# Kernel optimization log

Measured on AMD Instinct MI355X. Metric: run time of the kernel, lower is better.

## Reference

```python
import jax, jax.numpy as jnp
import numpy as np

B = 8192
D = 1024
NUM_CLASSES = 128
EPS = 1e-8  # torch F.cosine_similarity default eps


def setup_inputs() -> dict:
    key = jax.random.key(0)
    k1, k2, k3 = jax.random.split(key, 3)
    label_tensor = jax.random.randint(k1, (B,), 0, NUM_CLASSES, dtype=jnp.int64 if jax.config.jax_enable_x64 else jnp.int32)
    feature_a = jax.random.normal(k2, (B, D), dtype=jnp.float32)
    feature_b = jax.random.normal(k3, (B, D), dtype=jnp.float32)
    return {"label_tensor": label_tensor, "feature_a": feature_a, "feature_b": feature_b}


def reference(label_tensor, feature_a, feature_b):
    # Pairwise cosine similarity: cos_score[i, k] = cos(a_i, b_k), shape [B, B]
    dots = feature_a @ feature_b.T  # [B, B]
    na = jnp.linalg.norm(feature_a, axis=1)  # [B]
    nb = jnp.linalg.norm(feature_b, axis=1)  # [B]
    cos_score = dots / jnp.maximum(na[:, None] * nb[None, :], EPS)
    # Row-softmax (torch softmax dim=1 on the [B, B] matrix)
    logp = jax.nn.log_softmax(cos_score, axis=1)
    # Label-equality mask: positives for row i are all j with same label
    mask = (label_tensor[:, None] == label_tensor[None, :]).astype(cos_score.dtype)  # [B, B]
    per_row = -(mask * logp).sum(axis=1) / mask.sum(axis=1)  # diagonal guarantees >=1 positive
    loss = per_row.mean()
    return loss, cos_score
```

## Files before the change

### kernel.cpp

```cpp
#include <hip/hip_runtime.h>
#include <hip/hip_bf16.h>

#define NB 8192
#define ND 1024

typedef __bf16 bf16x8 __attribute__((ext_vector_type(8)));
typedef float  f32x4  __attribute__((ext_vector_type(4)));

__device__ inline void gload_lds16(const void* g, void* l) {
    __builtin_amdgcn_global_load_lds(
        (const __attribute__((address_space(1))) unsigned int*)g,
        (__attribute__((address_space(3))) unsigned int*)l,
        16, 0, 0);
}

__device__ inline unsigned short f2bf(float x) {
    unsigned int u = __float_as_uint(x);
    return (unsigned short)((u + 0x7fffu + ((u >> 16) & 1u)) >> 16);
}

#define BARRIER() asm volatile("s_barrier" ::: "memory")
#define VMCNT4()  asm volatile("s_waitcnt vmcnt(4)" ::: "memory")
#define VMCNT0()  asm volatile("s_waitcnt vmcnt(0)" ::: "memory")

__global__ __launch_bounds__(256) void prep_kernel(
    const float* __restrict__ A, const float* __restrict__ Bm,
    unsigned short* __restrict__ wa, unsigned short* __restrict__ wb,
    float* __restrict__ na, float* __restrict__ nb)
{
    int b = blockIdx.x;
    int wid = threadIdx.x >> 6, lane = threadIdx.x & 63;
    const float* src; unsigned short* dst; float* nrm; int row;
    if (b < 2048) { src = A;  dst = wa; nrm = na; row = b * 4 + wid; }
    else          { src = Bm; dst = wb; nrm = nb; row = (b - 2048) * 4 + wid; }

    const float*    rp = src + (size_t)row * ND;
    unsigned short* wp = dst + (size_t)row * ND;

    float ss = 0.f;
#pragma unroll
    for (int t = 0; t < 4; ++t) {
        int c = lane * 4 + t * 256;
        float4 v = *reinterpret_cast<const float4*>(rp + c);
        ss += v.x * v.x + v.y * v.y + v.z * v.z + v.w * v.w;
        ushort4 u;
        u.x = f2bf(v.x); u.y = f2bf(v.y); u.z = f2bf(v.z); u.w = f2bf(v.w);
        *reinterpret_cast<ushort4*>(wp + c) = u;
    }
#pragma unroll
    for (int off = 32; off; off >>= 1) ss += __shfl_xor(ss, off);
    if (lane == 0) nrm[row] = sqrtf(ss);
}

__global__ __launch_bounds__(256) void hist_kernel(
    const int* __restrict__ labels, int* __restrict__ hist)
{
    __shared__ int h[128];
    int tid = threadIdx.x;
    if (tid < 128) h[tid] = 0;
    __syncthreads();
    for (int i = tid; i < NB; i += 256) atomicAdd(&h[labels[i]], 1);
    __syncthreads();
    if (tid < 128) hist[tid] = h[tid];
}

__global__ __launch_bounds__(256) void gemm_cos(
    const unsigned short* __restrict__ wa, const unsigned short* __restrict__ wb,
    const float* __restrict__ na, const float* __restrict__ nb,
    const int* __restrict__ labels,
    float* __restrict__ C, float* __restrict__ pe, float* __restrict__ pm)
{
    __shared__ unsigned short lds[24576];

    const int bid = blockIdx.x;
    const int tm  = (bid & 7) * 8 + ((bid >> 3) & 7);
    const int tn  = bid >> 6;

    const int tid  = threadIdx.x;
    const int lane = tid & 63;
    const int wid  = tid >> 6;
    const int wr   = wid >> 1, wc = wid & 1;
    const int l15  = lane & 15, lg = lane >> 4;

    const int m0 = tm * 128, n0 = tn * 128;

    const int srow = tid >> 2;
    const int sg   = (tid & 3) ^ ((tid >> 3) & 3);
    const unsigned short* pA0 = wa + (size_t)(m0 + srow) * ND + sg * 8;
    const unsigned short* pA1 = pA0 + 64 * ND;
    const unsigned short* pB0 = wb + (size_t)(n0 + srow) * ND + sg * 8;
    const unsigned short* pB1 = pB0 + 64 * ND;
    const int stW = wid * 512;

    const int kg  = (lg ^ ((lane >> 1) & 3)) * 8;
    const int rdA = wr * 2048 + l15 * 32 + kg;
    const int rdB = 4096 + wc * 2048 + l15 * 32 + kg;

    f32x4 acc[4][4];
#pragma unroll
    for (int i = 0; i < 4; ++i)
#pragma unroll
        for (int j = 0; j < 4; ++j) acc[i][j] = (f32x4){0.f, 0.f, 0.f, 0.f};

#define STAGE(t, BUF) do { \
    gload_lds16(pA0 + (t) * 32, &lds[(BUF) + stW]); \
    gload_lds16(pA1 + (t) * 32, &lds[(BUF) + 2048 + stW]); \
    gload_lds16(pB0 + (t) * 32, &lds[(BUF) + 4096 + stW]); \
    gload_lds16(pB1 + (t) * 32, &lds[(BUF) + 6144 + stW]); } while (0)

#define COMPUTE(BUF) do { \
    bf16x8 bq[4], af[4]; \
    _Pragma("unroll") \
    for (int n_ = 0; n_ < 4; ++n_) \
        bq[n_] = *reinterpret_cast<const bf16x8*>(&lds[(BUF) + rdB + n_ * 512]); \
    _Pragma("unroll") \
    for (int m_ = 0; m_ < 4; ++m_) \
        af[m_] = *reinterpret_cast<const bf16x8*>(&lds[(BUF) + rdA + m_ * 512]); \
    _Pragma("unroll") \
    for (int m_ = 0; m_ < 4; ++m_) \
        _Pragma("unroll") \
        for (int n_ = 0; n_ < 4; ++n_) \
            acc[m_][n_] = __builtin_amdgcn_mfma_f32_16x16x32_bf16( \
                af[m_], bq[n_], acc[m_][n_], 0, 0, 0); \
    } while (0)

    STAGE(0, 0);
    STAGE(1, 8192);
    VMCNT4();
    BARRIER();

#pragma unroll
    for (int t = 0; t < 32; ++t) {
        const int cb  = (t % 3) * 8192;
        const int nb2 = ((t + 2) % 3) * 8192;
        if (t < 30) STAGE(t + 2, nb2);
        COMPUTE(cb);
        if (t < 29)      VMCNT4();
        else if (t < 31) VMCNT0();
        BARRIER();
    }

#undef COMPUTE
#undef STAGE

    __syncthreads();
    float* pl = reinterpret_cast<float*>(lds);

    float nbv[4]; int labc[4];
#pragma unroll
    for (int n = 0; n < 4; ++n) {
        int c = n0 + wc * 64 + n * 16 + l15;
        nbv[n] = nb[c]; labc[n] = labels[c];
    }

#pragma unroll
    for (int m = 0; m < 4; ++m) {
#pragma unroll
        for (int jj = 0; jj < 4; ++jj) {
            int rl = wr * 64 + m * 16 + lg * 4 + jj;
            int r  = m0 + rl;
            float nav = na[r]; int labr = labels[r];
            float es = 0.f, ms = 0.f;
#pragma unroll
            for (int n = 0; n < 4; ++n) {
                int c = n0 + wc * 64 + n * 16 + l15;
                float v = acc[m][n][jj] / fmaxf(nav * nbv[n], 1e-8f);
                C[(size_t)r * NB + c] = v;
                es += __expf(v);
                ms += (labc[n] == labr) ? v : 0.f;
            }
#pragma unroll
            for (int off = 1; off < 16; off <<= 1) {
                es += __shfl_xor(es, off);
                ms += __shfl_xor(ms, off);
            }
            if (l15 == 0) {
                int o = rl * 4 + wc * 2;
                pl[o] = es; pl[o + 1] = ms;
            }
        }
    }
    __syncthreads();
    if (tid < 128) {
        float es = pl[tid * 4]     + pl[tid * 4 + 2];
        float ms = pl[tid * 4 + 1] + pl[tid * 4 + 3];
        pe[tn * NB + m0 + tid] = es;
        pm[tn * NB + m0 + tid] = ms;
    }
}

__global__ __launch_bounds__(256) void loss_final(
    const float* __restrict__ pe, const float* __restrict__ pm,
    const int* __restrict__ labels, const int* __restrict__ hist,
    float* __restrict__ per_row)
{
    int row = blockIdx.x * 256 + threadIdx.x;
    float es = 0.f, ms = 0.f;
#pragma unroll
    for (int t = 0; t < 64; ++t) {
        es += pe[t * NB + row];
        ms += pm[t * NB + row];
    }
    per_row[row] = logf(es) - ms / (float)hist[labels[row]];
}

__global__ __launch_bounds__(256) void finalize(
    const float* __restrict__ per_row, float* __restrict__ out)
{
    __shared__ float sm[256];
    float s = 0.f;
    for (int i = threadIdx.x; i < NB; i += 256) s += per_row[i];
    sm[threadIdx.x] = s;
    __syncthreads();
    for (int k = 128; k; k >>= 1) {
        if (threadIdx.x < k) sm[threadIdx.x] += sm[threadIdx.x + k];
        __syncthreads();
    }
    if (threadIdx.x == 0) out[0] = sm[0] * (1.0f / (float)NB);
}

extern "C" void kernel_launch(void* const* d_in, const int* in_sizes, int n_in,
                              void* d_out, int out_size, void* d_ws, size_t ws_size,
                              hipStream_t stream) {
    const int*   labels = (const int*)d_in[0];
    const float* A      = (const float*)d_in[1];
    const float* Bm     = (const float*)d_in[2];
    float* out = (float*)d_out;

    char* ws = (char*)d_ws;
    unsigned short* wa = (unsigned short*)(ws);
    unsigned short* wb = (unsigned short*)(ws + 16777216);
    float* na      = (float*)(ws + 33554432);
    float* nb      = (float*)(ws + 33554432 + 32768);
    float* per_row = (float*)(ws + 33554432 + 65536);
    int*   hist    = (int*)  (ws + 33554432 + 98304);
    float* pe      = (float*)(ws + 33554432 + 131072);
    float* pm      = (float*)(ws + 33554432 + 131072 + 2097152);

    float* cosm = out + 1;

    prep_kernel<<<4096, 256, 0, stream>>>(A, Bm, wa, wb, na, nb);
    hist_kernel<<<1,    256, 0, stream>>>(labels, hist);
    gemm_cos   <<<4096, 256, 0, stream>>>(wa, wb, na, nb, labels, cosm, pe, pm);
    loss_final <<<32,   256, 0, stream>>>(pe, pm, labels, hist, per_row);
    finalize   <<<1,    256, 0, stream>>>(per_row, out);
}
```

Before: 271.7 us.

## Load B operand directly into registers from fragment-major pre-swizzled layout

The prep kernel now writes the bf16 copy of feature_b in a fragment-major layout that matches the MFMA B-operand, with 16-row by 8-element groups. The GEMM loads B fragments straight from global memory into double-buffered registers instead of staging them through LDS. Only A still goes through the triple-buffered LDS pipeline, which halves the shared-memory footprint. This removes the LDS writes and reads for B and may raise occupancy. In exchange, each wave issues redundant global loads for B that are shared across wave rows, and it relies on inline-asm waitcnt accounting.

```diff
diff --git a/kernel.cpp b/kernel.cpp
--- a/kernel.cpp
+++ b/kernel.cpp
@@ -5,6 +5,7 @@
 #define ND 1024
 
 typedef __bf16 bf16x8 __attribute__((ext_vector_type(8)));
+typedef int    i32x4  __attribute__((ext_vector_type(4)));
 typedef float  f32x4  __attribute__((ext_vector_type(4)));
 
 __device__ inline void gload_lds16(const void* g, void* l) {
@@ -14,28 +15,31 @@
         16, 0, 0);
 }
 
+__device__ inline void bload(const unsigned short* p, i32x4& d) {
+    asm volatile("global_load_dwordx4 %0, %1, off"
+                 : "=v"(d) : "v"(p) : "memory");
+}
+
 __device__ inline unsigned short f2bf(float x) {
     unsigned int u = __float_as_uint(x);
     return (unsigned short)((u + 0x7fffu + ((u >> 16) & 1u)) >> 16);
 }
 
 #define BARRIER() asm volatile("s_barrier" ::: "memory")
-#define VMCNT4()  asm volatile("s_waitcnt vmcnt(4)" ::: "memory")
+#define VMCNT6()  asm volatile("s_waitcnt vmcnt(6)" ::: "memory")
 #define VMCNT0()  asm volatile("s_waitcnt vmcnt(0)" ::: "memory")
+#define LGKM0()   asm volatile("s_waitcnt lgkmcnt(0)" ::: "memory")
 
 __global__ __launch_bounds__(256) void prep_kernel(
     const float* __restrict__ A, const float* __restrict__ Bm,
-    unsigned short* __restrict__ wa, unsigned short* __restrict__ wb,
+    unsigned short* __restrict__ wa, unsigned short* __restrict__ wb2,
     float* __restrict__ na, float* __restrict__ nb)
 {
     int b = blockIdx.x;
     int wid = threadIdx.x >> 6, lane = threadIdx.x & 63;
-    const float* src; unsigned short* dst; float* nrm; int row;
-    if (b < 2048) { src = A;  dst = wa; nrm = na; row = b * 4 + wid; }
-    else          { src = Bm; dst = wb; nrm = nb; row = (b - 2048) * 4 + wid; }
-
-    const float*    rp = src + (size_t)row * ND;
-    unsigned short* wp = dst + (size_t)row * ND;
+    bool isA = (b < 2048);
+    int row = (isA ? b : b - 2048) * 4 + wid;
+    const float* rp = (isA ? A : Bm) + (size_t)row * ND;
 
     float ss = 0.f;
 #pragma unroll
@@ -45,11 +49,17 @@
         ss += v.x * v.x + v.y * v.y + v.z * v.z + v.w * v.w;
         ushort4 u;
         u.x = f2bf(v.x); u.y = f2bf(v.y); u.z = f2bf(v.z); u.w = f2bf(v.w);
-        *reinterpret_cast<ushort4*>(wp + c) = u;
+        if (isA) {
+            *reinterpret_cast<ushort4*>(wa + (size_t)row * ND + c) = u;
+        } else {
+            size_t idx = (size_t)(row >> 4) * 16384 + (c >> 3) * 128
+                       + (row & 15) * 8 + (c & 7);
+            *reinterpret_cast<ushort4*>(wb2 + idx) = u;
+        }
     }
 #pragma unroll
     for (int off = 32; off; off >>= 1) ss += __shfl_xor(ss, off);
-    if (lane == 0) nrm[row] = sqrtf(ss);
+    if (lane == 0) (isA ? na : nb)[row] = sqrtf(ss);
 }
 
 __global__ __launch_bounds__(256) void hist_kernel(
@@ -65,12 +75,12 @@
 }
 
 __global__ __launch_bounds__(256) void gemm_cos(
-    const unsigned short* __restrict__ wa, const unsigned short* __restrict__ wb,
+    const unsigned short* __restrict__ wa, const unsigned short* __restrict__ wb2,
     const float* __restrict__ na, const float* __restrict__ nb,
     const int* __restrict__ labels,
     float* __restrict__ C, float* __restrict__ pe, float* __restrict__ pm)
 {
-    __shared__ unsigned short lds[24576];
+    __shared__ unsigned short lds[12288];
 
     const int bid = blockIdx.x;
     const int tm  = (bid & 7) * 8 + ((bid >> 3) & 7);
@@ -88,13 +98,13 @@
     const int sg   = (tid & 3) ^ ((tid >> 3) & 3);
     const unsigned short* pA0 = wa + (size_t)(m0 + srow) * ND + sg * 8;
     const unsigned short* pA1 = pA0 + 64 * ND;
-    const unsigned short* pB0 = wb + (size_t)(n0 + srow) * ND + sg * 8;
-    const unsigned short* pB1 = pB0 + 64 * ND;
     const int stW = wid * 512;
 
     const int kg  = (lg ^ ((lane >> 1) & 3)) * 8;
     const int rdA = wr * 2048 + l15 * 32 + kg;
-    const int rdB = 4096 + wc * 2048 + l15 * 32 + kg;
+
+    const unsigned short* qB = wb2 + (size_t)tn * 131072 + wc * 65536
+                             + lg * 128 + l15 * 8;
 
     f32x4 acc[4][4];
 #pragma unroll
@@ -102,46 +112,49 @@
 #pragma unroll
         for (int j = 0; j < 4; ++j) acc[i][j] = (f32x4){0.f, 0.f, 0.f, 0.f};
 
-#define STAGE(t, BUF) do { \
+    i32x4 breg[2][4];
+
+#define STAGE_A(t, BUF) do { \
     gload_lds16(pA0 + (t) * 32, &lds[(BUF) + stW]); \
-    gload_lds16(pA1 + (t) * 32, &lds[(BUF) + 2048 + stW]); \
-    gload_lds16(pB0 + (t) * 32, &lds[(BUF) + 4096 + stW]); \
-    gload_lds16(pB1 + (t) * 32, &lds[(BUF) + 6144 + stW]); } while (0)
-
-#define COMPUTE(BUF) do { \
-    bf16x8 bq[4], af[4]; \
-    _Pragma("unroll") \
+    gload_lds16(pA1 + (t) * 32, &lds[(BUF) + 2048 + stW]); } while (0)
+
+#define BLOAD(t, P) do { _Pragma("unroll") \
     for (int n_ = 0; n_ < 4; ++n_) \
-        bq[n_] = *reinterpret_cast<const bf16x8*>(&lds[(BUF) + rdB + n_ * 512]); \
-    _Pragma("unroll") \
-    for (int m_ = 0; m_ < 4; ++m_) \
-        af[m_] = *reinterpret_cast<const bf16x8*>(&lds[(BUF) + rdA + m_ * 512]); \
-    _Pragma("unroll") \
-    for (int m_ = 0; m_ < 4; ++m_) \
-        _Pragma("unroll") \
-        for (int n_ = 0; n_ < 4; ++n_) \
-            acc[m_][n_] = __builtin_amdgcn_mfma_f32_16x16x32_bf16( \
-                af[m_], bq[n_], acc[m_][n_], 0, 0, 0); \
-    } while (0)
-
-    STAGE(0, 0);
-    STAGE(1, 8192);
-    VMCNT4();
+        bload(qB + (t) * 512 + n_ * 16384, breg[P][n_]); } while (0)
+
+    STAGE_A(0, 0);
+    STAGE_A(1, 4096);
+    BLOAD(0, 0);
+    VMCNT6();
     BARRIER();
 
 #pragma unroll
     for (int t = 0; t < 32; ++t) {
-        const int cb  = (t % 3) * 8192;
-        const int nb2 = ((t + 2) % 3) * 8192;
-        if (t < 30) STAGE(t + 2, nb2);
-        COMPUTE(cb);
-        if (t < 29)      VMCNT4();
-        else if (t < 31) VMCNT0();
+        const int cb  = (t % 3) * 4096;
+        const int nb2 = ((t + 2) % 3) * 4096;
+        const int cp  = t & 1, np = cp ^ 1;
+        if (t < 30) STAGE_A(t + 2, nb2);
+        if (t < 31) BLOAD(t + 1, np);
+        bf16x8 af[4];
+#pragma unroll
+        for (int m_ = 0; m_ < 4; ++m_)
+            af[m_] = *reinterpret_cast<const bf16x8*>(&lds[cb + rdA + m_ * 512]);
+        if (t < 31) VMCNT6();
+        else        VMCNT0();
+        __builtin_amdgcn_sched_barrier(0);
+#pragma unroll
+        for (int m_ = 0; m_ < 4; ++m_)
+#pragma unroll
+            for (int n_ = 0; n_ < 4; ++n_)
+                acc[m_][n_] = __builtin_amdgcn_mfma_f32_16x16x32_bf16(
+                    af[m_], __builtin_bit_cast(bf16x8, breg[cp][n_]),
+                    acc[m_][n_], 0, 0, 0);
+        LGKM0();
         BARRIER();
     }
 
-#undef COMPUTE
-#undef STAGE
+#undef BLOAD
+#undef STAGE_A
 
     __syncthreads();
     float* pl = reinterpret_cast<float*>(lds);
@@ -228,8 +241,8 @@
     float* out = (float*)d_out;
 
     char* ws = (char*)d_ws;
-    unsigned short* wa = (unsigned short*)(ws);
-    unsigned short* wb = (unsigned short*)(ws + 16777216);
+    unsigned short* wa  = (unsigned short*)(ws);
+    unsigned short* wb2 = (unsigned short*)(ws + 16777216);
     float* na      = (float*)(ws + 33554432);
     float* nb      = (float*)(ws + 33554432 + 32768);
     float* per_row = (float*)(ws + 33554432 + 65536);
@@ -239,9 +252,9 @@
 
     float* cosm = out + 1;
 
-    prep_kernel<<<4096, 256, 0, stream>>>(A, Bm, wa, wb, na, nb);
+    prep_kernel<<<4096, 256, 0, stream>>>(A, Bm, wa, wb2, na, nb);
     hist_kernel<<<1,    256, 0, stream>>>(labels, hist);
-    gemm_cos   <<<4096, 256, 0, stream>>>(wa, wb, na, nb, labels, cosm, pe, pm);
+    gemm_cos   <<<4096, 256, 0, stream>>>(wa, wb2, na, nb, labels, cosm, pe, pm);
     loss_final <<<32,   256, 0, stream>>>(pe, pm, labels, hist, per_row);
     finalize   <<<1,    256, 0, stream>>>(per_row, out);
 }
```

Result: slower. 295.4 us (+8.7%).

## Switch GEMM mainloop to K=64 tiles with double buffering and XOR swizzle

Applied to the files above, without the earlier changes.

The GEMM K-step grows from 32 to 64, so each stage loads 8 direct-to-LDS chunks per thread into a 64-wide swizzled layout and each compute does two MFMA k-substeps. The 3-stage ring with vmcnt(4) is replaced by a 2-stage double buffer that waits on vmcnt(0) and lgkmcnt(0) every iteration. The aim is to halve the number of barriers and loop iterations and to reduce LDS bank conflicts with an 8-way XOR swizzle. The trade-off is less prefetch depth (one stage ahead instead of two) and more LDS use (64 KB), which may cut occupancy and expose memory latency.

```diff
diff --git a/kernel.cpp b/kernel.cpp
--- a/kernel.cpp
+++ b/kernel.cpp
@@ -20,8 +20,8 @@
 }
 
 #define BARRIER() asm volatile("s_barrier" ::: "memory")
-#define VMCNT4()  asm volatile("s_waitcnt vmcnt(4)" ::: "memory")
 #define VMCNT0()  asm volatile("s_waitcnt vmcnt(0)" ::: "memory")
+#define LGKM0()   asm volatile("s_waitcnt lgkmcnt(0)" ::: "memory")
 
 __global__ __launch_bounds__(256) void prep_kernel(
     const float* __restrict__ A, const float* __restrict__ Bm,
@@ -70,7 +70,7 @@
     const int* __restrict__ labels,
     float* __restrict__ C, float* __restrict__ pe, float* __restrict__ pm)
 {
-    __shared__ unsigned short lds[24576];
+    __shared__ unsigned short lds[32768];
 
     const int bid = blockIdx.x;
     const int tm  = (bid & 7) * 8 + ((bid >> 3) & 7);
@@ -84,17 +84,15 @@
 
     const int m0 = tm * 128, n0 = tn * 128;
 
-    const int srow = tid >> 2;
-    const int sg   = (tid & 3) ^ ((tid >> 3) & 3);
-    const unsigned short* pA0 = wa + (size_t)(m0 + srow) * ND + sg * 8;
-    const unsigned short* pA1 = pA0 + 64 * ND;
-    const unsigned short* pB0 = wb + (size_t)(n0 + srow) * ND + sg * 8;
-    const unsigned short* pB1 = pB0 + 64 * ND;
+    const int srow = tid >> 3;
+    const int sgr  = (tid & 7) ^ (srow & 7);
+    const unsigned short* pA = wa + (size_t)(m0 + srow) * ND + sgr * 8;
+    const unsigned short* pB = wb + (size_t)(n0 + srow) * ND + sgr * 8;
     const int stW = wid * 512;
 
-    const int kg  = (lg ^ ((lane >> 1) & 3)) * 8;
-    const int rdA = wr * 2048 + l15 * 32 + kg;
-    const int rdB = 4096 + wc * 2048 + l15 * 32 + kg;
+    const int kg = (lg ^ (l15 & 7)) * 8;
+    const int bA = (wr * 64 + l15) * 64 + kg;
+    const int bB = 8192 + (wc * 64 + l15) * 64 + kg;
 
     f32x4 acc[4][4];
 #pragma unroll
@@ -103,40 +101,47 @@
         for (int j = 0; j < 4; ++j) acc[i][j] = (f32x4){0.f, 0.f, 0.f, 0.f};
 
 #define STAGE(t, BUF) do { \
-    gload_lds16(pA0 + (t) * 32, &lds[(BUF) + stW]); \
-    gload_lds16(pA1 + (t) * 32, &lds[(BUF) + 2048 + stW]); \
-    gload_lds16(pB0 + (t) * 32, &lds[(BUF) + 4096 + stW]); \
-    gload_lds16(pB1 + (t) * 32, &lds[(BUF) + 6144 + stW]); } while (0)
+    _Pragma("unroll") \
+    for (int c_ = 0; c_ < 4; ++c_) { \
+        gload_lds16(pA + (size_t)c_ * 32 * ND + (t) * 64, \
+                    &lds[(BUF) + c_ * 2048 + stW]); \
+        gload_lds16(pB + (size_t)c_ * 32 * ND + (t) * 64, \
+                    &lds[(BUF) + 8192 + c_ * 2048 + stW]); \
+    } } while (0)
 
 #define COMPUTE(BUF) do { \
-    bf16x8 bq[4], af[4]; \
     _Pragma("unroll") \
-    for (int n_ = 0; n_ < 4; ++n_) \
-        bq[n_] = *reinterpret_cast<const bf16x8*>(&lds[(BUF) + rdB + n_ * 512]); \
-    _Pragma("unroll") \
-    for (int m_ = 0; m_ < 4; ++m_) \
-        af[m_] = *reinterpret_cast<const bf16x8*>(&lds[(BUF) + rdA + m_ * 512]); \
-    _Pragma("unroll") \
-    for (int m_ = 0; m_ < 4; ++m_) \
+    for (int ks_ = 0; ks_ < 2; ++ks_) { \
+        const int kx = ks_ * 32; \
+        bf16x8 bq[4], af[4]; \
         _Pragma("unroll") \
         for (int n_ = 0; n_ < 4; ++n_) \
-            acc[m_][n_] = __builtin_amdgcn_mfma_f32_16x16x32_bf16( \
-                af[m_], bq[n_], acc[m_][n_], 0, 0, 0); \
-    } while (0)
+            bq[n_] = *reinterpret_cast<const bf16x8*>( \
+                &lds[(BUF) + ((bB + n_ * 1024) ^ kx)]); \
+        _Pragma("unroll") \
+        for (int m_ = 0; m_ < 4; ++m_) \
+            af[m_] = *reinterpret_cast<const bf16x8*>( \
+                &lds[(BUF) + ((bA + m_ * 1024) ^ kx)]); \
+        _Pragma("unroll") \
+        for (int m_ = 0; m_ < 4; ++m_) \
+            _Pragma("unroll") \
+            for (int n_ = 0; n_ < 4; ++n_) \
+                acc[m_][n_] = __builtin_amdgcn_mfma_f32_16x16x32_bf16( \
+                    af[m_], bq[n_], acc[m_][n_], 0, 0, 0); \
+    } } while (0)
 
     STAGE(0, 0);
-    STAGE(1, 8192);
-    VMCNT4();
+    VMCNT0();
     BARRIER();
 
 #pragma unroll
-    for (int t = 0; t < 32; ++t) {
-        const int cb  = (t % 3) * 8192;
-        const int nb2 = ((t + 2) % 3) * 8192;
-        if (t < 30) STAGE(t + 2, nb2);
+    for (int t = 0; t < 16; ++t) {
+        const int cb = (t & 1) * 16384;
+        if (t < 15) STAGE(t + 1, cb ^ 16384);
         COMPUTE(cb);
-        if (t < 29)      VMCNT4();
-        else if (t < 31) VMCNT0();
+        __builtin_amdgcn_sched_barrier(0);
+        VMCNT0();
+        LGKM0();
         BARRIER();
     }
 
```

New measurement: 274.5 us. About the same (+1.0%).

## Split A/B staging with asymmetric buffering to cut LDS and raise occupancy

Applied to the files above, without the earlier changes.

The GEMM pipeline now stages A tiles with three buffers (two tiles ahead) and B tiles with only two buffers (one tile ahead), shrinking shared memory from 48KB to 40KB per block. Launch bounds request 4 blocks per CU, and the wait counts are adjusted, adding an explicit LDS-counter wait before each barrier. The aim is higher occupancy to hide memory latency. The cost is less prefetch depth for B, so B loads have less time to land before they are used.

```diff
diff --git a/kernel.cpp b/kernel.cpp
--- a/kernel.cpp
+++ b/kernel.cpp
@@ -20,8 +20,9 @@
 }
 
 #define BARRIER() asm volatile("s_barrier" ::: "memory")
-#define VMCNT4()  asm volatile("s_waitcnt vmcnt(4)" ::: "memory")
+#define VMCNT2()  asm volatile("s_waitcnt vmcnt(2)" ::: "memory")
 #define VMCNT0()  asm volatile("s_waitcnt vmcnt(0)" ::: "memory")
+#define LGKM0()   asm volatile("s_waitcnt lgkmcnt(0)" ::: "memory")
 
 __global__ __launch_bounds__(256) void prep_kernel(
     const float* __restrict__ A, const float* __restrict__ Bm,
@@ -64,13 +65,13 @@
     if (tid < 128) hist[tid] = h[tid];
 }
 
-__global__ __launch_bounds__(256) void gemm_cos(
+__global__ __launch_bounds__(256, 4) void gemm_cos(
     const unsigned short* __restrict__ wa, const unsigned short* __restrict__ wb,
     const float* __restrict__ na, const float* __restrict__ nb,
     const int* __restrict__ labels,
     float* __restrict__ C, float* __restrict__ pe, float* __restrict__ pm)
 {
-    __shared__ unsigned short lds[24576];
+    __shared__ unsigned short lds[20480];
 
     const int bid = blockIdx.x;
     const int tm  = (bid & 7) * 8 + ((bid >> 3) & 7);
@@ -94,7 +95,7 @@
 
     const int kg  = (lg ^ ((lane >> 1) & 3)) * 8;
     const int rdA = wr * 2048 + l15 * 32 + kg;
-    const int rdB = 4096 + wc * 2048 + l15 * 32 + kg;
+    const int rdB = wc * 2048 + l15 * 32 + kg;
 
     f32x4 acc[4][4];
 #pragma unroll
@@ -102,20 +103,22 @@
 #pragma unroll
         for (int j = 0; j < 4; ++j) acc[i][j] = (f32x4){0.f, 0.f, 0.f, 0.f};
 
-#define STAGE(t, BUF) do { \
+#define STAGE_A(t, BUF) do { \
     gload_lds16(pA0 + (t) * 32, &lds[(BUF) + stW]); \
-    gload_lds16(pA1 + (t) * 32, &lds[(BUF) + 2048 + stW]); \
-    gload_lds16(pB0 + (t) * 32, &lds[(BUF) + 4096 + stW]); \
-    gload_lds16(pB1 + (t) * 32, &lds[(BUF) + 6144 + stW]); } while (0)
-
-#define COMPUTE(BUF) do { \
+    gload_lds16(pA1 + (t) * 32, &lds[(BUF) + 2048 + stW]); } while (0)
+
+#define STAGE_B(t, BUF) do { \
+    gload_lds16(pB0 + (t) * 32, &lds[(BUF) + stW]); \
+    gload_lds16(pB1 + (t) * 32, &lds[(BUF) + 2048 + stW]); } while (0)
+
+#define COMPUTE(ABUF, BBUF) do { \
     bf16x8 bq[4], af[4]; \
     _Pragma("unroll") \
     for (int n_ = 0; n_ < 4; ++n_) \
-        bq[n_] = *reinterpret_cast<const bf16x8*>(&lds[(BUF) + rdB + n_ * 512]); \
+        bq[n_] = *reinterpret_cast<const bf16x8*>(&lds[(BBUF) + rdB + n_ * 512]); \
     _Pragma("unroll") \
     for (int m_ = 0; m_ < 4; ++m_) \
-        af[m_] = *reinterpret_cast<const bf16x8*>(&lds[(BUF) + rdA + m_ * 512]); \
+        af[m_] = *reinterpret_cast<const bf16x8*>(&lds[(ABUF) + rdA + m_ * 512]); \
     _Pragma("unroll") \
     for (int m_ = 0; m_ < 4; ++m_) \
         _Pragma("unroll") \
@@ -124,24 +127,28 @@
                 af[m_], bq[n_], acc[m_][n_], 0, 0, 0); \
     } while (0)
 
-    STAGE(0, 0);
-    STAGE(1, 8192);
-    VMCNT4();
+    STAGE_A(0, 0);
+    STAGE_B(0, 12288);
+    STAGE_A(1, 4096);
+    VMCNT2();
     BARRIER();
 
 #pragma unroll
     for (int t = 0; t < 32; ++t) {
-        const int cb  = (t % 3) * 8192;
-        const int nb2 = ((t + 2) % 3) * 8192;
-        if (t < 30) STAGE(t + 2, nb2);
-        COMPUTE(cb);
-        if (t < 29)      VMCNT4();
-        else if (t < 31) VMCNT0();
+        const int ab = (t % 3) * 4096;
+        const int bb = 12288 + (t & 1) * 4096;
+        if (t < 31) STAGE_B(t + 1, 12288 + ((t + 1) & 1) * 4096);
+        if (t < 30) STAGE_A(t + 2, ((t + 2) % 3) * 4096);
+        COMPUTE(ab, bb);
+        if (t < 30) VMCNT2();
+        else        VMCNT0();
+        LGKM0();
         BARRIER();
     }
 
 #undef COMPUTE
-#undef STAGE
+#undef STAGE_B
+#undef STAGE_A
 
     __syncthreads();
     float* pl = reinterpret_cast<float*>(lds);
```

After: 285.4 us. 1.05x slower.
